# Kernel tuning notes

Hardware: AMD Instinct MI355X
Metric: run time of the kernel (lower is better)

## Reference

```python
import jax, jax.numpy as jnp
import numpy as np

B, N, D = 4, 2048, 512
H = 8
E = D // H  # head_size = 64


def setup_inputs() -> dict:
    key = jax.random.key(0)
    ks = jax.random.split(key, 7)
    x1 = jax.random.normal(ks[0], (B, N, D), dtype=jnp.float32)  # keys
    x2 = jax.random.normal(ks[1], (B, N, D), dtype=jnp.float32)  # queries
    v = jax.random.normal(ks[2], (B, N, D), dtype=jnp.float32)
    # Conv1d(kernel_size=1, bias=False) weights per head, squeezed to matrices.
    s = 0.02
    Wq = jax.random.normal(ks[3], (H, E, D), dtype=jnp.float32) * s  # [head, head_size, q_feat]
    Wk = jax.random.normal(ks[4], (H, E, D), dtype=jnp.float32) * s
    Wv = jax.random.normal(ks[5], (H, E, D), dtype=jnp.float32) * s
    Wo = jax.random.normal(ks[6], (H, D, E), dtype=jnp.float32) * s  # [head, out_size, head_size]
    return {"x1": x1, "x2": x2, "v": v, "Wq": Wq, "Wk": Wk, "Wv": Wv, "Wo": Wo}


def reference(x1, x2, v, Wq, Wk, Wv, Wo):
    # rep='identity': k = x1, q = x2
    # Per-head 1x1 conv projections, vectorized over heads.
    Qh = jnp.einsum('bnd,hed->bhne', x2, Wq)   # [B,H,N,E]
    Kh = jnp.einsum('bnd,hed->bhne', x1, Wk)
    Vh = jnp.einsum('bnd,hed->bhne', v, Wv)
    scale = jnp.sqrt(jnp.float32(E))
    scores = jnp.einsum('bhie,bhje->bhij', Qh, Kh) / scale  # [B,H,Nq,Nk]
    weights = jax.nn.softmax(scores, axis=-1)
    rep_h = jnp.einsum('bhij,bhje->bhie', weights, Vh)       # [B,H,Nq,E]
    # Per-head output projection, summed over heads (rep += output_layers[h](...)).
    out = jnp.einsum('bhie,hoe->bio', rep_h, Wo)             # [B,Nq,out_size]
    return out
```

## Files before the change

### kernel.cpp

```cpp
#include <hip/hip_runtime.h>
#include <math.h>

#define NN 2048
#define DD 512
#define HH 8
#define EE 64

typedef unsigned short u16;
typedef __attribute__((ext_vector_type(8))) short bf16x8;
typedef __attribute__((ext_vector_type(4))) float f32x4;

#define MFMA(a,b,c) __builtin_amdgcn_mfma_f32_16x16x32_bf16((a),(b),(c),0,0,0)

__device__ __forceinline__ float fexp2(float x){
#if __has_builtin(__builtin_amdgcn_exp2f)
  return __builtin_amdgcn_exp2f(x);
#else
  return exp2f(x);
#endif
}

__device__ __forceinline__ unsigned rnd1(float x){
  unsigned u = __float_as_uint(x);
  return (u + 0x7fffu + ((u >> 16) & 1u)) >> 16;
}
__device__ __forceinline__ unsigned pk2(float a, float b){
  return rnd1(a) | (rnd1(b) << 16);
}
union I4V { int4 i; bf16x8 v; };
__device__ __forceinline__ bf16x8 ld_frag(const u16* p){
  I4V u; u.i = *(const int4*)p; return u.v;
}
__device__ __forceinline__ bf16x8 mk_frag(int a, int b, int c, int d){
  I4V u; u.i = make_int4(a,b,c,d); return u.v;
}


__global__ __launch_bounds__(256) void precvt_kernel(
    const float* __restrict__ Wq, const float* __restrict__ Wk,
    const float* __restrict__ Wv, const float* __restrict__ Wo,
    u16* __restrict__ wpk, u16* __restrict__ wopk)
{
  const int tid = blockIdx.x * 256 + threadIdx.x;
  const int seg = blockIdx.y;
  const int lane = tid & 63, jl = lane & 15, q = lane >> 4;
  const int es = (tid >> 6) & 3, kc = (tid >> 8) & 15, hh = tid >> 12;

  if (seg < 3) {
    const float* Wsrc = (seg == 0) ? Wq : (seg == 1) ? Wk : Wv;
    const float s = (seg == 0) ? 0.18033688011112042f : 1.0f;
    const float* src = Wsrc + ((size_t)hh * 64 + es * 16 + jl) * DD + kc * 32 + q * 8;
    float4 fa = *(const float4*)src;
    float4 fb = *(const float4*)(src + 4);
    int4 pk = make_int4(pk2(fa.x*s, fa.y*s), pk2(fa.z*s, fa.w*s),
                        pk2(fb.x*s, fb.y*s), pk2(fb.z*s, fb.w*s));
    *(int4*)&wpk[(size_t)(((seg*8 + hh)*16 + kc)*4 + es)*512 + lane*8] = pk;
  } else {
    const int k = kc * 32 + q * 8;
    const float* src = Wo + ((size_t)(k >> 6) * DD + hh * 64 + es * 16 + jl) * EE + (k & 63);
    float4 fa = *(const float4*)src;
    float4 fb = *(const float4*)(src + 4);
    int4 pk = make_int4(pk2(fa.x, fa.y), pk2(fa.z, fa.w),
                        pk2(fb.x, fb.y), pk2(fb.z, fb.w));
    *(int4*)&wopk[(size_t)(((hh*16 + kc)*4 + es)*512) + lane*8] = pk;
  }
}

__global__ __launch_bounds__(256) void xpack_kernel(
    const float* __restrict__ x1, const float* __restrict__ x2,
    const float* __restrict__ vin, u16* __restrict__ xpk)
{
  __shared__ float lds[64][68];
  const int nt = blockIdx.x, dt = blockIdx.y, pb = blockIdx.z;
  const int p = pb >> 2, b = pb & 3;
  const float* X = (p == 0) ? x2 : (p == 1) ? x1 : vin;
  const int t = threadIdx.x;

  {
    const int r = t >> 2, c0 = (t & 3) * 16;
    const float* src = X + ((size_t)b * NN + nt * 64 + r) * DD + dt * 64 + c0;
    float4 f0 = ((const float4*)src)[0];
    float4 f1 = ((const float4*)src)[1];
    float4 f2 = ((const float4*)src)[2];
    float4 f3 = ((const float4*)src)[3];
    *(float4*)&lds[r][c0]      = f0;
    *(float4*)&lds[r][c0 + 4]  = f1;
    *(float4*)&lds[r][c0 + 8]  = f2;
    *(float4*)&lds[r][c0 + 12] = f3;
  }
  __syncthreads();

  const int lane = t & 63, w = t >> 6, jl = lane & 15, q = lane >> 4;
  #pragma unroll
  for (int kcl = 0; kcl < 2; ++kcl) {
    float4 fa = *(const float4*)&lds[w * 16 + jl][kcl * 32 + q * 8];
    float4 fb = *(const float4*)&lds[w * 16 + jl][kcl * 32 + q * 8 + 4];
    int4 pk = make_int4(pk2(fa.x, fa.y), pk2(fa.z, fa.w),
                        pk2(fb.x, fb.y), pk2(fb.z, fb.w));
    const int ng = nt * 4 + w, kc = dt * 2 + kcl;
    *(int4*)&xpk[((((size_t)pb * 128 + ng) * 16 + kc) * 64 + lane) * 8] = pk;
  }
}

__global__ __launch_bounds__(256) void qkvproj_kernel(
    const u16* __restrict__ xpk, const u16* __restrict__ wpk,
    u16* __restrict__ Qpk, u16* __restrict__ Kpk, u16* __restrict__ Vpk)
{
  const int t = threadIdx.x, w = t >> 6, lane = t & 63;
  const int jl = lane & 15, q = lane >> 4;
  const int bn = blockIdx.x, ph = blockIdx.y;
  const int b = bn >> 5, nt = bn & 31, p = ph >> 3, h = ph & 7;

  const u16* xb = xpk + (((size_t)(p * 4 + b) * 128 + nt * 4 + w) * 16) * 512;
  const u16* wb = wpk + (size_t)ph * 32768;

  f32x4 acc[4];
  #pragma unroll
  for (int i = 0; i < 4; ++i) acc[i] = (f32x4){0.f,0.f,0.f,0.f};

  #pragma unroll 4
  for (int kc = 0; kc < 16; ++kc) {
    bf16x8 xf = ld_frag(xb + kc * 512 + lane * 8);
    #pragma unroll
    for (int es = 0; es < 4; ++es) {
      bf16x8 wf = ld_frag(wb + (size_t)(kc * 4 + es) * 512 + lane * 8);
      acc[es] = MFMA(wf, xf, acc[es]);
    }
  }

  const int bh = b * 8 + h;
  if (p < 2) {
    u16* O = (p ? Kpk : Qpk) + (size_t)bh * 131072;
    const int ng = nt * 4 + w;
    #pragma unroll
    for (int es = 0; es < 4; ++es) {
      const int kh = es >> 1, qp = (es & 1) * 2 + (q >> 1), off = (q & 1) * 4;
      *(uint2*)&O[(size_t)((ng * 2 + kh) * 64 + qp * 16 + jl) * 8 + off] =
          make_uint2(pk2(acc[es][0], acc[es][1]), pk2(acc[es][2], acc[es][3]));
    }
  } else {
    u16* O = Vpk + (size_t)bh * 131072 + nt * 4096;
    const int jc = w >> 1, qp = (w & 1) * 2 + (jl >> 3), jj = jl & 7;
    #pragma unroll
    for (int es = 0; es < 4; ++es)
      #pragma unroll
      for (int r = 0; r < 4; ++r)
        O[(size_t)((jc * 4 + es) * 64 + qp * 16 + q * 4 + r) * 8 + jj] =
            (u16)rnd1(acc[es][r]);
  }
}

__global__ __launch_bounds__(256, 2) void attn_kernel(
    const u16* __restrict__ Qpk, const u16* __restrict__ Kpk,
    const u16* __restrict__ Vpk, u16* __restrict__ Rpk)
{
  __shared__ union {
    short P[4][64][76];
    float slab[2][64 * 65];
  } sh;
  __shared__ float lbuf[4][64];

  const int tid = threadIdx.x, w = tid >> 6, lane = tid & 63;
  const int jl = lane & 15, q = lane >> 4;
  const int bx = blockIdx.x;
  const int itile = bx >> 5;
  const int bh = bx & 31;
  const int b = bh >> 3, h = bh & 7;

  bf16x8 qf[4][2];
  #pragma unroll
  for (int is = 0; is < 4; ++is)
    #pragma unroll
    for (int kh = 0; kh < 2; ++kh)
      qf[is][kh] = ld_frag(Qpk + ((size_t)bh * 128 + itile * 4 + is) * 1024
                           + kh * 512 + lane * 8);

  const u16* Kp = Kpk + (size_t)bh * 131072 + (size_t)w * 32 * 1024;
  const u16* Vp = Vpk + (size_t)bh * 131072 + (size_t)w * 8 * 4096;

  char* pw = (char*)&sh.P[0][0][0] + w * 9728 + jl * 152 + q * 8;
  const char* pr = (const char*)&sh.P[0][0][0] + w * 9728 + jl * 152 + q * 16;

  f32x4 acc[4][4];
  #pragma unroll
  for (int m = 0; m < 4; ++m)
    #pragma unroll
    for (int e = 0; e < 4; ++e) acc[m][e] = (f32x4){0.f,0.f,0.f,0.f};
  float lac[4] = {0.f, 0.f, 0.f, 0.f};

  for (int jt = 0; jt < 8; ++jt) {
    #pragma unroll
    for (int jm = 0; jm < 4; ++jm) {
      bf16x8 k0 = ld_frag(Kp + (jt * 4 + jm) * 1024 + lane * 8);
      bf16x8 k1 = ld_frag(Kp + (jt * 4 + jm) * 1024 + 512 + lane * 8);
      #pragma unroll
      for (int is = 0; is < 4; ++is) {
        f32x4 c = (f32x4){0.f,0.f,0.f,0.f};
        c = MFMA(k0, qf[is][0], c);
        c = MFMA(k1, qf[is][1], c);
        float e0 = fexp2(c[0]), e1 = fexp2(c[1]);
        float e2 = fexp2(c[2]), e3 = fexp2(c[3]);
        lac[is] += (e0 + e1) + (e2 + e3);
        int2 pv; pv.x = pk2(e0, e1); pv.y = pk2(e2, e3);
        *(int2*)(pw + is * 2432 + jm * 32) = pv;
      }
    }
    const u16* Vb = Vp + jt * 4096;
    bf16x8 vf[4][2];
    #pragma unroll
    for (int es = 0; es < 4; ++es) {
      vf[es][0] = ld_frag(Vb + es * 512 + lane * 8);
      vf[es][1] = ld_frag(Vb + 2048 + es * 512 + lane * 8);
    }
    #pragma unroll
    for (int m = 0; m < 4; ++m) {
      int2 a0 = *(const int2*)(pr + m * 2432);
      int2 a1 = *(const int2*)(pr + m * 2432 + 8);
      int2 a2 = *(const int2*)(pr + m * 2432 + 64);
      int2 a3 = *(const int2*)(pr + m * 2432 + 72);
      bf16x8 p0 = mk_frag(a0.x, a0.y, a1.x, a1.y);
      bf16x8 p1 = mk_frag(a2.x, a2.y, a3.x, a3.y);
      #pragma unroll
      for (int es = 0; es < 4; ++es) {
        acc[m][es] = MFMA(p0, vf[es][0], acc[m][es]);
        acc[m][es] = MFMA(p1, vf[es][1], acc[m][es]);
      }
    }
  }

  #pragma unroll
  for (int is = 0; is < 4; ++is) {
    float lv = lac[is];
    lv += __shfl_xor(lv, 16, 64);
    lv += __shfl_xor(lv, 32, 64);
    if (lane < 16) lbuf[w][is * 16 + lane] = lv;
  }
  __syncthreads();

  if (w >= 2) {
    float* s = sh.slab[w - 2];
    #pragma unroll
    for (int m = 0; m < 4; ++m)
      #pragma unroll
      for (int es = 0; es < 4; ++es)
        #pragma unroll
        for (int r = 0; r < 4; ++r)
          s[(m * 16 + q * 4 + r) * 65 + es * 16 + jl] = acc[m][es][r];
  }
  __syncthreads();
  if (w < 2) {
    const float* s = sh.slab[w];
    #pragma unroll
    for (int m = 0; m < 4; ++m)
      #pragma unroll
      for (int es = 0; es < 4; ++es)
        #pragma unroll
        for (int r = 0; r < 4; ++r)
          acc[m][es][r] += s[(m * 16 + q * 4 + r) * 65 + es * 16 + jl];
  }
  __syncthreads();
  if (w == 1) {
    float* s = sh.slab[0];
    #pragma unroll
    for (int m = 0; m < 4; ++m)
      #pragma unroll
      for (int es = 0; es < 4; ++es)
        #pragma unroll
        for (int r = 0; r < 4; ++r)
          s[(m * 16 + q * 4 + r) * 65 + es * 16 + jl] = acc[m][es][r];
  }
  __syncthreads();
  if (w == 0) {
    const float* s = sh.slab[0];
    #pragma unroll
    for (int m = 0; m < 4; ++m) {
      float il[4];
      #pragma unroll
      for (int r = 0; r < 4; ++r) {
        const int i = m * 16 + q * 4 + r;
        il[r] = 1.0f / (lbuf[0][i] + lbuf[1][i] + lbuf[2][i] + lbuf[3][i]);
      }
      const int rg = b * 128 + itile * 4 + m;
      #pragma unroll
      for (int es = 0; es < 4; ++es) {
        const int kc = h * 2 + (es >> 1);
        const int qp = (es & 1) * 2 + (jl >> 3), jj = jl & 7;
        #pragma unroll
        for (int r = 0; r < 4; ++r) {
          float val = (acc[m][es][r] + s[(m * 16 + q * 4 + r) * 65 + es * 16 + jl]) * il[r];
          Rpk[((size_t)rg * 16 + kc) * 512 + (size_t)(qp * 16 + q * 4 + r) * 8 + jj] =
              (u16)rnd1(val);
        }
      }
    }
  }
}

__global__ __launch_bounds__(256) void outproj_kernel(
    const u16* __restrict__ Rpk, const u16* __restrict__ wopk,
    float* __restrict__ out)
{
  const int t = threadIdx.x, w = t >> 6, lane = t & 63;
  const int jl = lane & 15, q = lane >> 4;
  const int rt = blockIdx.x, ot = blockIdx.y;
  const int rg = rt * 4 + w;

  f32x4 acc[4];
  #pragma unroll
  for (int i = 0; i < 4; ++i) acc[i] = (f32x4){0.f,0.f,0.f,0.f};

  #pragma unroll 4
  for (int kc = 0; kc < 16; ++kc) {
    bf16x8 bf = ld_frag(Rpk + ((size_t)rg * 16 + kc) * 512 + lane * 8);
    #pragma unroll
    for (int os = 0; os < 4; ++os) {
      bf16x8 wf = ld_frag(wopk + (size_t)((ot * 16 + kc) * 4 + os) * 512 + lane * 8);
      acc[os] = MFMA(wf, bf, acc[os]);
    }
  }

  #pragma unroll
  for (int os = 0; os < 4; ++os) {
    float4 o4 = make_float4(acc[os][0], acc[os][1], acc[os][2], acc[os][3]);
    *(float4*)&out[(size_t)(rt * 64 + w * 16 + jl) * DD + ot * 64 + os * 16 + q * 4] = o4;
  }
}

extern "C" void kernel_launch(void* const* d_in, const int* in_sizes, int n_in,
                              void* d_out, int out_size, void* d_ws, size_t ws_size,
                              hipStream_t stream)
{
  const float* x1 = (const float*)d_in[0];
  const float* x2 = (const float*)d_in[1];
  const float* vv = (const float*)d_in[2];
  const float* Wq = (const float*)d_in[3];
  const float* Wk = (const float*)d_in[4];
  const float* Wv = (const float*)d_in[5];
  const float* Wo = (const float*)d_in[6];
  float* out = (float*)d_out;

  char* W = (char*)d_ws;
  u16* wpk  = (u16*)(W);
  u16* wopk = (u16*)(W + 1572864);
  u16* xpk  = (u16*)(W + 2097152);
  u16* Qpk  = (u16*)(W + 27262976);
  u16* Kpk  = (u16*)(W + 35651584);
  u16* Vpk  = (u16*)(W + 44040192);
  u16* Rpk  = (u16*)(W + 52428800);

  precvt_kernel <<<dim3(128, 4), 256, 0, stream>>>(Wq, Wk, Wv, Wo, wpk, wopk);
  xpack_kernel  <<<dim3(32, 8, 12), 256, 0, stream>>>(x1, x2, vv, xpk);
  qkvproj_kernel<<<dim3(128, 24), 256, 0, stream>>>(xpk, wpk, Qpk, Kpk, Vpk);
  attn_kernel   <<<dim3(1024), 256, 0, stream>>>(Qpk, Kpk, Vpk, Rpk);
  outproj_kernel<<<dim3(128, 8), 256, 0, stream>>>(Rpk, wopk, out);
}
```

Baseline: 198.4 us.

## Loop heads in qkv projection, reload Q per tile, raise attn occupancy

The QKV projection now assigns four heads to each block and loops over them, reusing the same x tile and shrinking the grid from 3072 blocks to 768. The attention kernel reloads Q fragments inside the key-tile loop instead of keeping them in registers, and its launch bounds are raised so three blocks fit per CU. Probabilities are now packed to bf16 by truncation rather than rounding. The output projection grid is transposed so consecutive blocks share the same R rows. The trade-offs are fewer, longer projection blocks, repeated Q loads in attention, and slightly less accurate probability packing.

```diff
diff --git a/kernel.cpp b/kernel.cpp
--- a/kernel.cpp
+++ b/kernel.cpp
@@ -26,6 +26,9 @@
 }
 __device__ __forceinline__ unsigned pk2(float a, float b){
   return rnd1(a) | (rnd1(b) << 16);
+}
+__device__ __forceinline__ unsigned tpk2(float a, float b){
+  return (__float_as_uint(a) >> 16) | (__float_as_uint(b) & 0xffff0000u);
 }
 union I4V { int4 i; bf16x8 v; };
 __device__ __forceinline__ bf16x8 ld_frag(const u16* p){
@@ -108,49 +111,53 @@
 {
   const int t = threadIdx.x, w = t >> 6, lane = t & 63;
   const int jl = lane & 15, q = lane >> 4;
-  const int bn = blockIdx.x, ph = blockIdx.y;
-  const int b = bn >> 5, nt = bn & 31, p = ph >> 3, h = ph & 7;
+  const int p = blockIdx.x >> 1, hg = blockIdx.x & 1;
+  const int b = blockIdx.y >> 5, nt = blockIdx.y & 31;
 
   const u16* xb = xpk + (((size_t)(p * 4 + b) * 128 + nt * 4 + w) * 16) * 512;
-  const u16* wb = wpk + (size_t)ph * 32768;
-
-  f32x4 acc[4];
-  #pragma unroll
-  for (int i = 0; i < 4; ++i) acc[i] = (f32x4){0.f,0.f,0.f,0.f};
-
-  #pragma unroll 4
-  for (int kc = 0; kc < 16; ++kc) {
-    bf16x8 xf = ld_frag(xb + kc * 512 + lane * 8);
-    #pragma unroll
-    for (int es = 0; es < 4; ++es) {
-      bf16x8 wf = ld_frag(wb + (size_t)(kc * 4 + es) * 512 + lane * 8);
-      acc[es] = MFMA(wf, xf, acc[es]);
-    }
-  }
-
-  const int bh = b * 8 + h;
-  if (p < 2) {
-    u16* O = (p ? Kpk : Qpk) + (size_t)bh * 131072;
-    const int ng = nt * 4 + w;
-    #pragma unroll
-    for (int es = 0; es < 4; ++es) {
-      const int kh = es >> 1, qp = (es & 1) * 2 + (q >> 1), off = (q & 1) * 4;
-      *(uint2*)&O[(size_t)((ng * 2 + kh) * 64 + qp * 16 + jl) * 8 + off] =
-          make_uint2(pk2(acc[es][0], acc[es][1]), pk2(acc[es][2], acc[es][3]));
-    }
-  } else {
-    u16* O = Vpk + (size_t)bh * 131072 + nt * 4096;
-    const int jc = w >> 1, qp = (w & 1) * 2 + (jl >> 3), jj = jl & 7;
-    #pragma unroll
-    for (int es = 0; es < 4; ++es)
-      #pragma unroll
-      for (int r = 0; r < 4; ++r)
-        O[(size_t)((jc * 4 + es) * 64 + qp * 16 + q * 4 + r) * 8 + jj] =
-            (u16)rnd1(acc[es][r]);
-  }
-}
-
-__global__ __launch_bounds__(256, 2) void attn_kernel(
+
+  for (int hi = 0; hi < 4; ++hi) {
+    const int h = hg * 4 + hi;
+    const u16* wb = wpk + (size_t)(p * 8 + h) * 32768;
+
+    f32x4 acc[4];
+    #pragma unroll
+    for (int i = 0; i < 4; ++i) acc[i] = (f32x4){0.f,0.f,0.f,0.f};
+
+    #pragma unroll 4
+    for (int kc = 0; kc < 16; ++kc) {
+      bf16x8 xf = ld_frag(xb + kc * 512 + lane * 8);
+      #pragma unroll
+      for (int es = 0; es < 4; ++es) {
+        bf16x8 wf = ld_frag(wb + (size_t)(kc * 4 + es) * 512 + lane * 8);
+        acc[es] = MFMA(wf, xf, acc[es]);
+      }
+    }
+
+    const int bh = b * 8 + h;
+    if (p < 2) {
+      u16* O = (p ? Kpk : Qpk) + (size_t)bh * 131072;
+      const int ng = nt * 4 + w;
+      #pragma unroll
+      for (int es = 0; es < 4; ++es) {
+        const int kh = es >> 1, qp = (es & 1) * 2 + (q >> 1), off = (q & 1) * 4;
+        *(uint2*)&O[(size_t)((ng * 2 + kh) * 64 + qp * 16 + jl) * 8 + off] =
+            make_uint2(pk2(acc[es][0], acc[es][1]), pk2(acc[es][2], acc[es][3]));
+      }
+    } else {
+      u16* O = Vpk + (size_t)bh * 131072 + nt * 4096;
+      const int jc = w >> 1, qp = (w & 1) * 2 + (jl >> 3), jj = jl & 7;
+      #pragma unroll
+      for (int es = 0; es < 4; ++es)
+        #pragma unroll
+        for (int r = 0; r < 4; ++r)
+          O[(size_t)((jc * 4 + es) * 64 + qp * 16 + q * 4 + r) * 8 + jj] =
+              (u16)rnd1(acc[es][r]);
+    }
+  }
+}
+
+__global__ __launch_bounds__(256, 3) void attn_kernel(
     const u16* __restrict__ Qpk, const u16* __restrict__ Kpk,
     const u16* __restrict__ Vpk, u16* __restrict__ Rpk)
 {
@@ -167,16 +174,9 @@
   const int bh = bx & 31;
   const int b = bh >> 3, h = bh & 7;
 
-  bf16x8 qf[4][2];
-  #pragma unroll
-  for (int is = 0; is < 4; ++is)
-    #pragma unroll
-    for (int kh = 0; kh < 2; ++kh)
-      qf[is][kh] = ld_frag(Qpk + ((size_t)bh * 128 + itile * 4 + is) * 1024
-                           + kh * 512 + lane * 8);
-
-  const u16* Kp = Kpk + (size_t)bh * 131072 + (size_t)w * 32 * 1024;
-  const u16* Vp = Vpk + (size_t)bh * 131072 + (size_t)w * 8 * 4096;
+  const u16* Qp = Qpk + ((size_t)bh * 128 + itile * 4) * 1024;
+  const u16* Kp = Kpk + (size_t)bh * 131072 + (size_t)w * 32768;
+  const u16* Vp = Vpk + (size_t)bh * 131072 + (size_t)w * 32768;
 
   char* pw = (char*)&sh.P[0][0][0] + w * 9728 + jl * 152 + q * 8;
   const char* pr = (const char*)&sh.P[0][0][0] + w * 9728 + jl * 152 + q * 16;
@@ -189,6 +189,12 @@
   float lac[4] = {0.f, 0.f, 0.f, 0.f};
 
   for (int jt = 0; jt < 8; ++jt) {
+    bf16x8 qf[4][2];
+    #pragma unroll
+    for (int is = 0; is < 4; ++is) {
+      qf[is][0] = ld_frag(Qp + is * 1024 + lane * 8);
+      qf[is][1] = ld_frag(Qp + is * 1024 + 512 + lane * 8);
+    }
     #pragma unroll
     for (int jm = 0; jm < 4; ++jm) {
       bf16x8 k0 = ld_frag(Kp + (jt * 4 + jm) * 1024 + lane * 8);
@@ -201,7 +207,7 @@
         float e0 = fexp2(c[0]), e1 = fexp2(c[1]);
         float e2 = fexp2(c[2]), e3 = fexp2(c[3]);
         lac[is] += (e0 + e1) + (e2 + e3);
-        int2 pv; pv.x = pk2(e0, e1); pv.y = pk2(e2, e3);
+        int2 pv; pv.x = tpk2(e0, e1); pv.y = tpk2(e2, e3);
         *(int2*)(pw + is * 2432 + jm * 32) = pv;
       }
     }
@@ -302,7 +308,7 @@
 {
   const int t = threadIdx.x, w = t >> 6, lane = t & 63;
   const int jl = lane & 15, q = lane >> 4;
-  const int rt = blockIdx.x, ot = blockIdx.y;
+  const int ot = blockIdx.x, rt = blockIdx.y;
   const int rg = rt * 4 + w;
 
   f32x4 acc[4];
@@ -350,7 +356,7 @@
 
   precvt_kernel <<<dim3(128, 4), 256, 0, stream>>>(Wq, Wk, Wv, Wo, wpk, wopk);
   xpack_kernel  <<<dim3(32, 8, 12), 256, 0, stream>>>(x1, x2, vv, xpk);
-  qkvproj_kernel<<<dim3(128, 24), 256, 0, stream>>>(xpk, wpk, Qpk, Kpk, Vpk);
+  qkvproj_kernel<<<dim3(6, 128), 256, 0, stream>>>(xpk, wpk, Qpk, Kpk, Vpk);
   attn_kernel   <<<dim3(1024), 256, 0, stream>>>(Qpk, Kpk, Vpk, Rpk);
-  outproj_kernel<<<dim3(128, 8), 256, 0, stream>>>(Rpk, wopk, out);
-}
+  outproj_kernel<<<dim3(8, 128), 256, 0, stream>>>(Rpk, wopk, out);
+}
```

New measurement: 273.5 us. +37.9%, slower.
